# Optimization experiments

Hardware: AMD Instinct MI355X
Metric: run time of the kernel (lower is better)

Reference implementation:

```python
import jax, jax.numpy as jnp
import numpy as np

N = 50000       # nodes
E = 800000      # edges (avg degree 16)
NFEAT = 256
NHID = 32
NHEADS = 4
ALPHA = 0.2     # leaky relu slope


def setup_inputs() -> dict:
    key = jax.random.key(0)
    ks = jax.random.split(key, 7)
    x = jax.random.normal(ks[0], (N, NFEAT), dtype=jnp.float32)
    src = jax.random.randint(ks[1], (E,), 0, N, dtype=jnp.int32)
    dst = jax.random.randint(ks[2], (E,), 0, N, dtype=jnp.int32)
    Ws = jax.random.normal(ks[3], (NHEADS, NFEAT, NHID), dtype=jnp.float32) * 0.05
    As = jax.random.normal(ks[4], (NHEADS, 2 * NHID), dtype=jnp.float32) * 0.05
    Wo = jax.random.normal(ks[5], (NHID * NHEADS, NHID), dtype=jnp.float32) * 0.05
    Ao = jax.random.normal(ks[6], (2 * NHID,), dtype=jnp.float32) * 0.05
    return {"x": x, "src": src, "dst": dst, "Ws": Ws, "As": As, "Wo": Wo, "Ao": Ao}


def _gat_layer(h, src, dst, W, a, concat):
    # h: [N, F_in] -> project
    h = h @ W                          # [N, d]
    d = W.shape[1]
    hs = h[src]                        # [E, d] gather source feats
    hd = h[dst]                        # [E, d] gather neighbor feats
    # a . concat([hs, hd]) == hs @ a[:d] + hd @ a[d:]
    e = hs @ a[:d] + hd @ a[d:]        # [E]
    e = jnp.where(e > 0, e, ALPHA * e)  # leaky relu
    # segment softmax keyed on src
    m = jax.ops.segment_max(e, src, num_segments=N)    # [N]
    ex = jnp.exp(e - m[src])
    denom = jax.ops.segment_sum(ex, src, num_segments=N)  # [N]
    att = ex / denom[src]              # [E]
    # weighted neighbor aggregation (scatter-sum on src)
    h_prime = jax.ops.segment_sum(att[:, None] * hd, src, num_segments=N)  # [N, d]
    return jax.nn.elu(h_prime) if concat else h_prime


def reference(x, src, dst, Ws, As, Wo, Ao):
    heads = [_gat_layer(x, src, dst, Ws[i], As[i], concat=True) for i in range(NHEADS)]
    h = jnp.concatenate(heads, axis=1)                 # [N, nhid*nheads]
    out = jax.nn.elu(_gat_layer(h, src, dst, Wo, Ao, concat=False))  # [N, nhid]
    return out
```

## Files before the change

### kernel.cpp

```cpp
#include <hip/hip_runtime.h>
#include <hip/hip_fp16.h>
#include <math.h>

#define N_NODES 50000
#define N_EDGES 800000
#define NFEAT 256
#define NHID 32
#define NHEADS 4
#define ALPHA 0.2f
#define ELLCAP 64
#define ELLSH 6

#define GEMM1_BLKS ((N_NODES + 63) / 64)
#define FILL_BLKS ((N_EDGES + 255) / 256)

typedef _Float16 half8_t __attribute__((ext_vector_type(8)));
typedef float f32x4 __attribute__((ext_vector_type(4)));

__device__ __forceinline__ float elu_f(float x) {
    return x > 0.0f ? x : (__expf(x) - 1.0f);
}

__device__ __forceinline__ float wexp(float x) {
    float l = x > 0.0f ? x : ALPHA * x;
    return __expf(l);
}

__device__ __forceinline__ float h2f_bits(unsigned wd, int sh) {
    ushort b = (ushort)(wd >> sh);
    return __half2float(*(__half*)&b);
}

__global__ void k_prep(const float* __restrict__ Ws, const float* __restrict__ Wo,
                       ushort* __restrict__ Wt1, ushort* __restrict__ Wt2,
                       int* __restrict__ deg) {
    int idx = blockIdx.x * 256 + threadIdx.x;
    if (idx < 128 * 256) {
        int c = idx >> 8;
        int k = idx & 255;
        __half hv = __float2half(Ws[(c >> 5) * (NFEAT * NHID) + k * NHID + (c & 31)]);
        Wt1[idx] = *(ushort*)&hv;
    } else if (idx < 128 * 256 + 32 * 128) {
        int j = idx - 128 * 256;
        int c = j >> 7;
        int k = j & 127;
        __half hv = __float2half(Wo[k * NHID + c]);
        Wt2[j] = *(ushort*)&hv;
    }
    int z = idx - (128 * 256 + 32 * 128);
    if (z >= 0 && z < N_NODES) deg[z] = 0;
}

template <int K, int NTILES, bool AHALF, int NH>
__device__ __forceinline__ void gemm_body(const void* __restrict__ Ain,
                                          const ushort* __restrict__ Wt,
                                          const float* __restrict__ attn,
                                          __half* __restrict__ C,
                                          float* __restrict__ So,
                                          float* __restrict__ Si,
                                          int nrows, int bid) {
    constexpr int N = NTILES * 16;
    constexpr int BK = 32;
    constexpr int LDB = 40;

    __shared__ __align__(16) ushort Bs[N * LDB];

    int tid = threadIdx.x;
    int w = tid >> 6;
    int lane = tid & 63;
    int c = lane & 15;
    int quad = lane >> 4;
    int row0 = bid * 64 + w * 16;
    int gm = row0 + c;
    if (gm >= nrows) gm = nrows - 1;

    f32x4 acc[NTILES];
#pragma unroll
    for (int nt = 0; nt < NTILES; nt++)
#pragma unroll
        for (int i = 0; i < 4; i++) acc[nt][i] = 0.0f;

    float a_so[NTILES], a_si[NTILES];
#pragma unroll
    for (int nt = 0; nt < NTILES; nt++) {
        int h = nt >> 1;
        a_so[nt] = attn[h * 64 + (nt & 1) * 16 + c];
        a_si[nt] = attn[h * 64 + 32 + (nt & 1) * 16 + c];
    }

    for (int k0 = 0; k0 < K; k0 += BK) {
        if (tid < N * 2) {
            int r = tid >> 1;
            int part = tid & 1;
            const uint4* gp = (const uint4*)(Wt + (size_t)r * K + k0 + part * 16);
            uint4 v0 = gp[0];
            uint4 v1 = gp[1];
            uint4* lp = (uint4*)&Bs[r * LDB + part * 16];
            lp[0] = v0;
            lp[1] = v1;
        }
        __syncthreads();

        half8_t ahi, alo;
        if constexpr (AHALF) {
            ahi = *(const half8_t*)((const ushort*)Ain + (size_t)gm * K + k0 + quad * 8);
        } else {
            const float* ap = (const float*)Ain + (size_t)gm * K + k0 + quad * 8;
            float4 x0 = *(const float4*)ap;
            float4 x1 = *(const float4*)(ap + 4);
            float xa[8] = {x0.x, x0.y, x0.z, x0.w, x1.x, x1.y, x1.z, x1.w};
#pragma unroll
            for (int j = 0; j < 8; j++) {
                _Float16 h = (_Float16)xa[j];
                ahi[j] = h;
                alo[j] = (_Float16)(xa[j] - (float)h);
            }
        }
#pragma unroll
        for (int nt = 0; nt < NTILES; nt++) {
            half8_t b = *(const half8_t*)&Bs[(nt * 16 + c) * LDB + quad * 8];
            acc[nt] = __builtin_amdgcn_mfma_f32_16x16x32_f16(ahi, b, acc[nt], 0, 0, 0);
            if constexpr (!AHALF)
                acc[nt] = __builtin_amdgcn_mfma_f32_16x16x32_f16(alo, b, acc[nt], 0, 0, 0);
        }
        __syncthreads();
    }

#pragma unroll
    for (int reg = 0; reg < 4; reg++) {
        int ro = row0 + quad * 4 + reg;
        bool ok = ro < nrows;
        if (ok) {
#pragma unroll
            for (int nt = 0; nt < NTILES; nt++)
                C[(size_t)ro * N + nt * 16 + c] = __float2half(acc[nt][reg]);
        }
#pragma unroll
        for (int h = 0; h < NH; h++) {
            float so = acc[2 * h][reg] * a_so[2 * h] + acc[2 * h + 1][reg] * a_so[2 * h + 1];
            float si = acc[2 * h][reg] * a_si[2 * h] + acc[2 * h + 1][reg] * a_si[2 * h + 1];
            so += __shfl_xor(so, 1); si += __shfl_xor(si, 1);
            so += __shfl_xor(so, 2); si += __shfl_xor(si, 2);
            so += __shfl_xor(so, 4); si += __shfl_xor(si, 4);
            so += __shfl_xor(so, 8); si += __shfl_xor(si, 8);
            if (c == 0 && ok) {
                So[(size_t)ro * NH + h] = so;
                Si[(size_t)ro * NH + h] = si;
            }
        }
    }
}

__global__ __launch_bounds__(256) void k_g1fill(const float* __restrict__ x,
                                                const ushort* __restrict__ Wt1,
                                                const float* __restrict__ attn,
                                                __half* __restrict__ H1h,
                                                float* __restrict__ S1o,
                                                float* __restrict__ S1i,
                                                const int* __restrict__ src,
                                                const int* __restrict__ dst,
                                                int* __restrict__ deg,
                                                ushort* __restrict__ ell2) {
    if (blockIdx.x < GEMM1_BLKS) {
        gemm_body<256, 8, false, 4>(x, Wt1, attn, H1h, S1o, S1i, N_NODES, blockIdx.x);
    } else {
        int e = (blockIdx.x - GEMM1_BLKS) * 256 + threadIdx.x;
        if (e < N_EDGES) {
            int s = src[e];
            int v = dst[e];
            int slot = atomicAdd(&deg[s], 1);
            if (slot < ELLCAP) ell2[((size_t)s << ELLSH) + slot] = (ushort)v;
        }
    }
}

__global__ __launch_bounds__(256) void k_gemm2(const __half* __restrict__ Hch,
                                               const ushort* __restrict__ Wt2,
                                               const float* __restrict__ attn,
                                               __half* __restrict__ H2h,
                                               float* __restrict__ S2o,
                                               float* __restrict__ S2i) {
    gemm_body<128, 2, true, 1>(Hch, Wt2, attn, H2h, S2o, S2i, N_NODES, blockIdx.x);
}

__global__ __launch_bounds__(256) void k_aggw4(const int* __restrict__ deg,
                                               const ushort* __restrict__ ell2,
                                               const float* __restrict__ S1o,
                                               const float* __restrict__ S1i,
                                               const __half* __restrict__ H1h,
                                               __half* __restrict__ Hch) {
    __shared__ uint4 ew[4][ELLCAP];
    int wv = threadIdx.x >> 6;
    int node = blockIdx.x * 4 + wv;
    int lane = threadIdx.x & 63;
    int dg = deg[node];
    if (dg > ELLCAP) dg = ELLCAP;
    if (lane < dg) {
        int v = ell2[((size_t)node << ELLSH) + lane];
        float4 so = *(const float4*)(S1o + 4 * (size_t)node);
        float4 si = *(const float4*)(S1i + 4 * (size_t)v);
        __half2 w01 = __floats2half2_rn(wexp(so.x + si.x), wexp(so.y + si.y));
        __half2 w23 = __floats2half2_rn(wexp(so.z + si.z), wexp(so.w + si.w));
        uint4 q;
        q.x = (unsigned)v;
        q.y = *(unsigned*)&w01;
        q.z = *(unsigned*)&w23;
        q.w = 0;
        ew[wv][lane] = q;
    }
    __syncthreads();
    int sel = (lane >> 4) & 2;
    int sh = ((lane >> 4) & 1) * 16;
    const unsigned* Hp = (const unsigned*)H1h;
    float a0 = 0.0f, a1 = 0.0f, d = 0.0f;
    int j = 0;
    for (; j + 3 < dg; j += 4) {
        uint4 q0 = ew[wv][j];
        uint4 q1 = ew[wv][j + 1];
        uint4 q2 = ew[wv][j + 2];
        uint4 q3 = ew[wv][j + 3];
        unsigned u0 = Hp[((size_t)q0.x << 6) + lane];
        unsigned u1 = Hp[((size_t)q1.x << 6) + lane];
        unsigned u2 = Hp[((size_t)q2.x << 6) + lane];
        unsigned u3 = Hp[((size_t)q3.x << 6) + lane];
        float w0 = h2f_bits(sel ? q0.z : q0.y, sh);
        float w1 = h2f_bits(sel ? q1.z : q1.y, sh);
        float w2 = h2f_bits(sel ? q2.z : q2.y, sh);
        float w3 = h2f_bits(sel ? q3.z : q3.y, sh);
        float2 h0 = __half22float2(*(__half2*)&u0);
        float2 h1 = __half22float2(*(__half2*)&u1);
        float2 h2 = __half22float2(*(__half2*)&u2);
        float2 h3 = __half22float2(*(__half2*)&u3);
        a0 += w0 * h0.x; a1 += w0 * h0.y; d += w0;
        a0 += w1 * h1.x; a1 += w1 * h1.y; d += w1;
        a0 += w2 * h2.x; a1 += w2 * h2.y; d += w2;
        a0 += w3 * h3.x; a1 += w3 * h3.y; d += w3;
    }
    for (; j < dg; j++) {
        uint4 q0 = ew[wv][j];
        unsigned u0 = Hp[((size_t)q0.x << 6) + lane];
        float w0 = h2f_bits(sel ? q0.z : q0.y, sh);
        float2 h0 = __half22float2(*(__half2*)&u0);
        a0 += w0 * h0.x; a1 += w0 * h0.y; d += w0;
    }
    float inv = d > 0.0f ? 1.0f / d : 0.0f;
    __half2 o = __floats2half2_rn(elu_f(a0 * inv), elu_f(a1 * inv));
    *(__half2*)(Hch + ((size_t)node << 7) + 2 * lane) = o;
}

__global__ __launch_bounds__(256) void k_aggw2(const int* __restrict__ deg,
                                               const ushort* __restrict__ ell2,
                                               const float* __restrict__ S2o,
                                               const float* __restrict__ S2i,
                                               const __half* __restrict__ H2h,
                                               float* __restrict__ out) {
    __shared__ uint2 ew[16][ELLCAP];
    int t = blockIdx.x * 256 + threadIdx.x;
    int node = t >> 4;
    int ng = (threadIdx.x >> 4);
    int l = t & 15;
    int dg = deg[node];
    if (dg > ELLCAP) dg = ELLCAP;
    float so = S2o[node];
#pragma unroll
    for (int k = 0; k < 4; k++) {
        int j = l + k * 16;
        if (j < dg) {
            int v = ell2[((size_t)node << ELLSH) + j];
            float w = wexp(so + S2i[v]);
            uint2 q;
            q.x = (unsigned)v;
            q.y = __float_as_uint(w);
            ew[ng][j] = q;
        }
    }
    __syncthreads();
    const unsigned* Hp = (const unsigned*)H2h;
    float a0 = 0.0f, a1 = 0.0f, d = 0.0f;
    int j = 0;
    for (; j + 3 < dg; j += 4) {
        uint2 q0 = ew[ng][j];
        uint2 q1 = ew[ng][j + 1];
        uint2 q2 = ew[ng][j + 2];
        uint2 q3 = ew[ng][j + 3];
        unsigned u0 = Hp[((size_t)q0.x << 4) + l];
        unsigned u1 = Hp[((size_t)q1.x << 4) + l];
        unsigned u2 = Hp[((size_t)q2.x << 4) + l];
        unsigned u3 = Hp[((size_t)q3.x << 4) + l];
        float w0 = __uint_as_float(q0.y);
        float w1 = __uint_as_float(q1.y);
        float w2 = __uint_as_float(q2.y);
        float w3 = __uint_as_float(q3.y);
        float2 h0 = __half22float2(*(__half2*)&u0);
        float2 h1 = __half22float2(*(__half2*)&u1);
        float2 h2 = __half22float2(*(__half2*)&u2);
        float2 h3 = __half22float2(*(__half2*)&u3);
        a0 += w0 * h0.x; a1 += w0 * h0.y; d += w0;
        a0 += w1 * h1.x; a1 += w1 * h1.y; d += w1;
        a0 += w2 * h2.x; a1 += w2 * h2.y; d += w2;
        a0 += w3 * h3.x; a1 += w3 * h3.y; d += w3;
    }
    for (; j < dg; j++) {
        uint2 q0 = ew[ng][j];
        unsigned u0 = Hp[((size_t)q0.x << 4) + l];
        float w0 = __uint_as_float(q0.y);
        float2 h0 = __half22float2(*(__half2*)&u0);
        a0 += w0 * h0.x; a1 += w0 * h0.y; d += w0;
    }
    float inv = d > 0.0f ? 1.0f / d : 0.0f;
    float2 o = make_float2(elu_f(a0 * inv), elu_f(a1 * inv));
    *(float2*)(out + ((size_t)node << 5) + 2 * l) = o;
}

extern "C" void kernel_launch(void* const* d_in, const int* in_sizes, int n_in,
                              void* d_out, int out_size, void* d_ws, size_t ws_size,
                              hipStream_t stream) {
    const float* x = (const float*)d_in[0];
    const int* src = (const int*)d_in[1];
    const int* dst = (const int*)d_in[2];
    const float* Ws = (const float*)d_in[3];
    const float* As = (const float*)d_in[4];
    const float* Wo = (const float*)d_in[5];
    const float* Ao = (const float*)d_in[6];
    float* out = (float*)d_out;

    char* p = (char*)d_ws;
    auto alloc = [&](size_t bytes) -> void* {
        void* r = (void*)p;
        p += (bytes + 255) & ~(size_t)255;
        return r;
    };
    ushort* Wt1 = (ushort*)alloc((size_t)128 * 256 * 2);
    ushort* Wt2 = (ushort*)alloc((size_t)32 * 128 * 2);
    __half* H1h = (__half*)alloc((size_t)N_NODES * 128 * 2);
    __half* Hch = (__half*)alloc((size_t)N_NODES * 128 * 2);
    __half* H2h = (__half*)alloc((size_t)N_NODES * 32 * 2);
    float* S1o = (float*)alloc((size_t)N_NODES * 4 * 4);
    float* S1i = (float*)alloc((size_t)N_NODES * 4 * 4);
    float* S2o = (float*)alloc((size_t)N_NODES * 4);
    float* S2i = (float*)alloc((size_t)N_NODES * 4);
    int* deg   = (int*)alloc((size_t)N_NODES * 4);
    ushort* ell2 = (ushort*)alloc((size_t)N_NODES * ELLCAP * 2);

    const int PREP_THREADS = 128 * 256 + 32 * 128 + N_NODES;
    k_prep<<<(PREP_THREADS + 255) / 256, 256, 0, stream>>>(Ws, Wo, Wt1, Wt2, deg);

    k_g1fill<<<GEMM1_BLKS + FILL_BLKS, 256, 0, stream>>>(
        x, Wt1, As, H1h, S1o, S1i, src, dst, deg, ell2);

    k_aggw4<<<(N_NODES + 3) / 4, 256, 0, stream>>>(deg, ell2, S1o, S1i, H1h, Hch);

    k_gemm2<<<(N_NODES + 63) / 64, 256, 0, stream>>>(Hch, Wt2, Ao, H2h, S2o, S2i);

    k_aggw2<<<(N_NODES * 16 + 255) / 256, 256, 0, stream>>>(deg, ell2, S2o, S2i, H2h, out);
}
```

Measured before the change: 202.9 us.

## Replace global per-node ELL with 32-node edge buckets rebuilt in shared memory

Edge filling now appends packed (local node, neighbor) words into per-bucket lists of 32 source nodes, instead of doing an atomic and a 2-byte scattered write into a global per-node ELL. Each aggregation kernel loads one bucket, rebuilds the per-node neighbor lists in shared memory with LDS atomics, then processes its 32 nodes with waves or 16-lane groups looping over several nodes. The aim is to cut scattered global writes and global per-node atomics. The cost is heavier atomic contention on the bucket counters, the bucket-to-ELL rebuild being done twice, and fewer concurrent blocks with serial per-node loops in aggregation.

```diff
diff --git a/kernel.cpp b/kernel.cpp
--- a/kernel.cpp
+++ b/kernel.cpp
@@ -8,8 +8,11 @@
 #define NHID 32
 #define NHEADS 4
 #define ALPHA 0.2f
-#define ELLCAP 64
-#define ELLSH 6
+
+#define BSH 5
+#define BNODES 32
+#define NBUCK ((N_NODES + BNODES - 1) / BNODES)
+#define BCAP 704
 
 #define GEMM1_BLKS ((N_NODES + 63) / 64)
 #define FILL_BLKS ((N_EDGES + 255) / 256)
@@ -33,7 +36,7 @@
 
 __global__ void k_prep(const float* __restrict__ Ws, const float* __restrict__ Wo,
                        ushort* __restrict__ Wt1, ushort* __restrict__ Wt2,
-                       int* __restrict__ deg) {
+                       int* __restrict__ bcnt) {
     int idx = blockIdx.x * 256 + threadIdx.x;
     if (idx < 128 * 256) {
         int c = idx >> 8;
@@ -48,7 +51,7 @@
         Wt2[j] = *(ushort*)&hv;
     }
     int z = idx - (128 * 256 + 32 * 128);
-    if (z >= 0 && z < N_NODES) deg[z] = 0;
+    if (z >= 0 && z < NBUCK) bcnt[z] = 0;
 }
 
 template <int K, int NTILES, bool AHALF, int NH>
@@ -159,8 +162,8 @@
                                                 float* __restrict__ S1i,
                                                 const int* __restrict__ src,
                                                 const int* __restrict__ dst,
-                                                int* __restrict__ deg,
-                                                ushort* __restrict__ ell2) {
+                                                int* __restrict__ bcnt,
+                                                unsigned* __restrict__ bucket) {
     if (blockIdx.x < GEMM1_BLKS) {
         gemm_body<256, 8, false, 4>(x, Wt1, attn, H1h, S1o, S1i, N_NODES, blockIdx.x);
     } else {
@@ -168,8 +171,10 @@
         if (e < N_EDGES) {
             int s = src[e];
             int v = dst[e];
-            int slot = atomicAdd(&deg[s], 1);
-            if (slot < ELLCAP) ell2[((size_t)s << ELLSH) + slot] = (ushort)v;
+            int b = s >> BSH;
+            int pos = atomicAdd(&bcnt[b], 1);
+            if (pos < BCAP)
+                bucket[(size_t)b * BCAP + pos] = ((unsigned)(s & (BNODES - 1)) << 16) | (unsigned)v;
         }
     }
 }
@@ -183,133 +188,172 @@
     gemm_body<128, 2, true, 1>(Hch, Wt2, attn, H2h, S2o, S2i, N_NODES, blockIdx.x);
 }
 
-__global__ __launch_bounds__(256) void k_aggw4(const int* __restrict__ deg,
-                                               const ushort* __restrict__ ell2,
+__device__ __forceinline__ int build_ell(const int* __restrict__ bcnt,
+                                         const unsigned* __restrict__ bucket,
+                                         int b, int* ldeg, ushort* ell_l) {
+    int tid = threadIdx.x;
+    if (tid < BNODES) ldeg[tid] = 0;
+    __syncthreads();
+    int cnt = bcnt[b];
+    if (cnt > BCAP) cnt = BCAP;
+    const unsigned* bp = bucket + (size_t)b * BCAP;
+    for (int i = tid; i < cnt; i += 256) {
+        unsigned e = bp[i];
+        int sl = e >> 16;
+        int v = (int)(e & 0xFFFFu);
+        int slot = atomicAdd(&ldeg[sl], 1);
+        if (slot < 64) ell_l[(sl << 6) + slot] = (ushort)v;
+    }
+    __syncthreads();
+    return cnt;
+}
+
+__global__ __launch_bounds__(256) void k_agg1b(const int* __restrict__ bcnt,
+                                               const unsigned* __restrict__ bucket,
                                                const float* __restrict__ S1o,
                                                const float* __restrict__ S1i,
                                                const __half* __restrict__ H1h,
                                                __half* __restrict__ Hch) {
-    __shared__ uint4 ew[4][ELLCAP];
+    __shared__ int ldeg[BNODES];
+    __shared__ ushort ell_l[BNODES * 64];
+    __shared__ uint4 ew[4][64];
+    int b = blockIdx.x;
+    int base = b << BSH;
+    build_ell(bcnt, bucket, b, ldeg, ell_l);
+
     int wv = threadIdx.x >> 6;
-    int node = blockIdx.x * 4 + wv;
     int lane = threadIdx.x & 63;
-    int dg = deg[node];
-    if (dg > ELLCAP) dg = ELLCAP;
-    if (lane < dg) {
-        int v = ell2[((size_t)node << ELLSH) + lane];
-        float4 so = *(const float4*)(S1o + 4 * (size_t)node);
-        float4 si = *(const float4*)(S1i + 4 * (size_t)v);
-        __half2 w01 = __floats2half2_rn(wexp(so.x + si.x), wexp(so.y + si.y));
-        __half2 w23 = __floats2half2_rn(wexp(so.z + si.z), wexp(so.w + si.w));
-        uint4 q;
-        q.x = (unsigned)v;
-        q.y = *(unsigned*)&w01;
-        q.z = *(unsigned*)&w23;
-        q.w = 0;
-        ew[wv][lane] = q;
-    }
-    __syncthreads();
     int sel = (lane >> 4) & 2;
     int sh = ((lane >> 4) & 1) * 16;
     const unsigned* Hp = (const unsigned*)H1h;
-    float a0 = 0.0f, a1 = 0.0f, d = 0.0f;
-    int j = 0;
-    for (; j + 3 < dg; j += 4) {
-        uint4 q0 = ew[wv][j];
-        uint4 q1 = ew[wv][j + 1];
-        uint4 q2 = ew[wv][j + 2];
-        uint4 q3 = ew[wv][j + 3];
-        unsigned u0 = Hp[((size_t)q0.x << 6) + lane];
-        unsigned u1 = Hp[((size_t)q1.x << 6) + lane];
-        unsigned u2 = Hp[((size_t)q2.x << 6) + lane];
-        unsigned u3 = Hp[((size_t)q3.x << 6) + lane];
-        float w0 = h2f_bits(sel ? q0.z : q0.y, sh);
-        float w1 = h2f_bits(sel ? q1.z : q1.y, sh);
-        float w2 = h2f_bits(sel ? q2.z : q2.y, sh);
-        float w3 = h2f_bits(sel ? q3.z : q3.y, sh);
-        float2 h0 = __half22float2(*(__half2*)&u0);
-        float2 h1 = __half22float2(*(__half2*)&u1);
-        float2 h2 = __half22float2(*(__half2*)&u2);
-        float2 h3 = __half22float2(*(__half2*)&u3);
-        a0 += w0 * h0.x; a1 += w0 * h0.y; d += w0;
-        a0 += w1 * h1.x; a1 += w1 * h1.y; d += w1;
-        a0 += w2 * h2.x; a1 += w2 * h2.y; d += w2;
-        a0 += w3 * h3.x; a1 += w3 * h3.y; d += w3;
-    }
-    for (; j < dg; j++) {
-        uint4 q0 = ew[wv][j];
-        unsigned u0 = Hp[((size_t)q0.x << 6) + lane];
-        float w0 = h2f_bits(sel ? q0.z : q0.y, sh);
-        float2 h0 = __half22float2(*(__half2*)&u0);
-        a0 += w0 * h0.x; a1 += w0 * h0.y; d += w0;
-    }
-    float inv = d > 0.0f ? 1.0f / d : 0.0f;
-    __half2 o = __floats2half2_rn(elu_f(a0 * inv), elu_f(a1 * inv));
-    *(__half2*)(Hch + ((size_t)node << 7) + 2 * lane) = o;
-}
-
-__global__ __launch_bounds__(256) void k_aggw2(const int* __restrict__ deg,
-                                               const ushort* __restrict__ ell2,
+
+    for (int k = 0; k < 8; k++) {
+        int idx = wv + (k << 2);
+        int node = base + idx;
+        if (node >= N_NODES) continue;
+        int dg = ldeg[idx];
+        if (dg > 64) dg = 64;
+        if (lane < dg) {
+            int v = ell_l[(idx << 6) + lane];
+            float4 so = *(const float4*)(S1o + 4 * (size_t)node);
+            float4 si = *(const float4*)(S1i + 4 * (size_t)v);
+            __half2 w01 = __floats2half2_rn(wexp(so.x + si.x), wexp(so.y + si.y));
+            __half2 w23 = __floats2half2_rn(wexp(so.z + si.z), wexp(so.w + si.w));
+            uint4 q;
+            q.x = (unsigned)v;
+            q.y = *(unsigned*)&w01;
+            q.z = *(unsigned*)&w23;
+            q.w = 0;
+            ew[wv][lane] = q;
+        }
+        float a0 = 0.0f, a1 = 0.0f, d = 0.0f;
+        int j = 0;
+        for (; j + 3 < dg; j += 4) {
+            uint4 q0 = ew[wv][j];
+            uint4 q1 = ew[wv][j + 1];
+            uint4 q2 = ew[wv][j + 2];
+            uint4 q3 = ew[wv][j + 3];
+            unsigned u0 = Hp[((size_t)q0.x << 6) + lane];
+            unsigned u1 = Hp[((size_t)q1.x << 6) + lane];
+            unsigned u2 = Hp[((size_t)q2.x << 6) + lane];
+            unsigned u3 = Hp[((size_t)q3.x << 6) + lane];
+            float w0 = h2f_bits(sel ? q0.z : q0.y, sh);
+            float w1 = h2f_bits(sel ? q1.z : q1.y, sh);
+            float w2 = h2f_bits(sel ? q2.z : q2.y, sh);
+            float w3 = h2f_bits(sel ? q3.z : q3.y, sh);
+            float2 h0 = __half22float2(*(__half2*)&u0);
+            float2 h1 = __half22float2(*(__half2*)&u1);
+            float2 h2 = __half22float2(*(__half2*)&u2);
+            float2 h3 = __half22float2(*(__half2*)&u3);
+            a0 += w0 * h0.x; a1 += w0 * h0.y; d += w0;
+            a0 += w1 * h1.x; a1 += w1 * h1.y; d += w1;
+            a0 += w2 * h2.x; a1 += w2 * h2.y; d += w2;
+            a0 += w3 * h3.x; a1 += w3 * h3.y; d += w3;
+        }
+        for (; j < dg; j++) {
+            uint4 q0 = ew[wv][j];
+            unsigned u0 = Hp[((size_t)q0.x << 6) + lane];
+            float w0 = h2f_bits(sel ? q0.z : q0.y, sh);
+            float2 h0 = __half22float2(*(__half2*)&u0);
+            a0 += w0 * h0.x; a1 += w0 * h0.y; d += w0;
+        }
+        float inv = d > 0.0f ? 1.0f / d : 0.0f;
+        __half2 o = __floats2half2_rn(elu_f(a0 * inv), elu_f(a1 * inv));
+        *(__half2*)(Hch + ((size_t)node << 7) + 2 * lane) = o;
+    }
+}
+
+__global__ __launch_bounds__(256) void k_agg2b(const int* __restrict__ bcnt,
+                                               const unsigned* __restrict__ bucket,
                                                const float* __restrict__ S2o,
                                                const float* __restrict__ S2i,
                                                const __half* __restrict__ H2h,
                                                float* __restrict__ out) {
-    __shared__ uint2 ew[16][ELLCAP];
-    int t = blockIdx.x * 256 + threadIdx.x;
-    int node = t >> 4;
-    int ng = (threadIdx.x >> 4);
-    int l = t & 15;
-    int dg = deg[node];
-    if (dg > ELLCAP) dg = ELLCAP;
-    float so = S2o[node];
-#pragma unroll
-    for (int k = 0; k < 4; k++) {
-        int j = l + k * 16;
-        if (j < dg) {
-            int v = ell2[((size_t)node << ELLSH) + j];
-            float w = wexp(so + S2i[v]);
-            uint2 q;
-            q.x = (unsigned)v;
-            q.y = __float_as_uint(w);
-            ew[ng][j] = q;
-        }
-    }
-    __syncthreads();
+    __shared__ int ldeg[BNODES];
+    __shared__ ushort ell_l[BNODES * 64];
+    __shared__ uint2 ew2[16][64];
+    int b = blockIdx.x;
+    int base = b << BSH;
+    build_ell(bcnt, bucket, b, ldeg, ell_l);
+
+    int grp = threadIdx.x >> 4;
+    int l = threadIdx.x & 15;
     const unsigned* Hp = (const unsigned*)H2h;
-    float a0 = 0.0f, a1 = 0.0f, d = 0.0f;
-    int j = 0;
-    for (; j + 3 < dg; j += 4) {
-        uint2 q0 = ew[ng][j];
-        uint2 q1 = ew[ng][j + 1];
-        uint2 q2 = ew[ng][j + 2];
-        uint2 q3 = ew[ng][j + 3];
-        unsigned u0 = Hp[((size_t)q0.x << 4) + l];
-        unsigned u1 = Hp[((size_t)q1.x << 4) + l];
-        unsigned u2 = Hp[((size_t)q2.x << 4) + l];
-        unsigned u3 = Hp[((size_t)q3.x << 4) + l];
-        float w0 = __uint_as_float(q0.y);
-        float w1 = __uint_as_float(q1.y);
-        float w2 = __uint_as_float(q2.y);
-        float w3 = __uint_as_float(q3.y);
-        float2 h0 = __half22float2(*(__half2*)&u0);
-        float2 h1 = __half22float2(*(__half2*)&u1);
-        float2 h2 = __half22float2(*(__half2*)&u2);
-        float2 h3 = __half22float2(*(__half2*)&u3);
-        a0 += w0 * h0.x; a1 += w0 * h0.y; d += w0;
-        a0 += w1 * h1.x; a1 += w1 * h1.y; d += w1;
-        a0 += w2 * h2.x; a1 += w2 * h2.y; d += w2;
-        a0 += w3 * h3.x; a1 += w3 * h3.y; d += w3;
-    }
-    for (; j < dg; j++) {
-        uint2 q0 = ew[ng][j];
-        unsigned u0 = Hp[((size_t)q0.x << 4) + l];
-        float w0 = __uint_as_float(q0.y);
-        float2 h0 = __half22float2(*(__half2*)&u0);
-        a0 += w0 * h0.x; a1 += w0 * h0.y; d += w0;
-    }
-    float inv = d > 0.0f ? 1.0f / d : 0.0f;
-    float2 o = make_float2(elu_f(a0 * inv), elu_f(a1 * inv));
-    *(float2*)(out + ((size_t)node << 5) + 2 * l) = o;
+
+    for (int k = 0; k < 2; k++) {
+        int idx = grp + (k << 4);
+        int node = base + idx;
+        if (node >= N_NODES) continue;
+        int dg = ldeg[idx];
+        if (dg > 64) dg = 64;
+        float so = S2o[node];
+#pragma unroll
+        for (int q = 0; q < 4; q++) {
+            int j = l + (q << 4);
+            if (j < dg) {
+                int v = ell_l[(idx << 6) + j];
+                float w = wexp(so + S2i[v]);
+                uint2 qq;
+                qq.x = (unsigned)v;
+                qq.y = __float_as_uint(w);
+                ew2[grp][j] = qq;
+            }
+        }
+        float a0 = 0.0f, a1 = 0.0f, d = 0.0f;
+        int j = 0;
+        for (; j + 3 < dg; j += 4) {
+            uint2 q0 = ew2[grp][j];
+            uint2 q1 = ew2[grp][j + 1];
+            uint2 q2 = ew2[grp][j + 2];
+            uint2 q3 = ew2[grp][j + 3];
+            unsigned u0 = Hp[((size_t)q0.x << 4) + l];
+            unsigned u1 = Hp[((size_t)q1.x << 4) + l];
+            unsigned u2 = Hp[((size_t)q2.x << 4) + l];
+            unsigned u3 = Hp[((size_t)q3.x << 4) + l];
+            float w0 = __uint_as_float(q0.y);
+            float w1 = __uint_as_float(q1.y);
+            float w2 = __uint_as_float(q2.y);
+            float w3 = __uint_as_float(q3.y);
+            float2 h0 = __half22float2(*(__half2*)&u0);
+            float2 h1 = __half22float2(*(__half2*)&u1);
+            float2 h2 = __half22float2(*(__half2*)&u2);
+            float2 h3 = __half22float2(*(__half2*)&u3);
+            a0 += w0 * h0.x; a1 += w0 * h0.y; d += w0;
+            a0 += w1 * h1.x; a1 += w1 * h1.y; d += w1;
+            a0 += w2 * h2.x; a1 += w2 * h2.y; d += w2;
+            a0 += w3 * h3.x; a1 += w3 * h3.y; d += w3;
+        }
+        for (; j < dg; j++) {
+            uint2 q0 = ew2[grp][j];
+            unsigned u0 = Hp[((size_t)q0.x << 4) + l];
+            float w0 = __uint_as_float(q0.y);
+            float2 h0 = __half22float2(*(__half2*)&u0);
+            a0 += w0 * h0.x; a1 += w0 * h0.y; d += w0;
+        }
+        float inv = d > 0.0f ? 1.0f / d : 0.0f;
+        float2 o = make_float2(elu_f(a0 * inv), elu_f(a1 * inv));
+        *(float2*)(out + ((size_t)node << 5) + 2 * l) = o;
+    }
 }
 
 extern "C" void kernel_launch(void* const* d_in, const int* in_sizes, int n_in,
@@ -339,18 +383,18 @@
     float* S1i = (float*)alloc((size_t)N_NODES * 4 * 4);
     float* S2o = (float*)alloc((size_t)N_NODES * 4);
     float* S2i = (float*)alloc((size_t)N_NODES * 4);
-    int* deg   = (int*)alloc((size_t)N_NODES * 4);
-    ushort* ell2 = (ushort*)alloc((size_t)N_NODES * ELLCAP * 2);
-
-    const int PREP_THREADS = 128 * 256 + 32 * 128 + N_NODES;
-    k_prep<<<(PREP_THREADS + 255) / 256, 256, 0, stream>>>(Ws, Wo, Wt1, Wt2, deg);
+    int* bcnt = (int*)alloc((size_t)NBUCK * 4);
+    unsigned* bucket = (unsigned*)alloc((size_t)NBUCK * BCAP * 4);
+
+    const int PREP_THREADS = 128 * 256 + 32 * 128 + NBUCK;
+    k_prep<<<(PREP_THREADS + 255) / 256, 256, 0, stream>>>(Ws, Wo, Wt1, Wt2, bcnt);
 
     k_g1fill<<<GEMM1_BLKS + FILL_BLKS, 256, 0, stream>>>(
-        x, Wt1, As, H1h, S1o, S1i, src, dst, deg, ell2);
-
-    k_aggw4<<<(N_NODES + 3) / 4, 256, 0, stream>>>(deg, ell2, S1o, S1i, H1h, Hch);
+        x, Wt1, As, H1h, S1o, S1i, src, dst, bcnt, bucket);
+
+    k_agg1b<<<NBUCK, 256, 0, stream>>>(bcnt, bucket, S1o, S1i, H1h, Hch);
 
     k_gemm2<<<(N_NODES + 63) / 64, 256, 0, stream>>>(Hch, Wt2, Ao, H2h, S2o, S2i);
 
-    k_aggw2<<<(N_NODES * 16 + 255) / 256, 256, 0, stream>>>(deg, ell2, S2o, S2i, H2h, out);
-}
+    k_agg2b<<<NBUCK, 256, 0, stream>>>(bcnt, bucket, S2o, S2i, H2h, out);
+}
```

After: 269.7 us. 1.33x slower.
